# Kernel tuning notes

Measured on AMD Instinct MI355X. Metric: run time of the kernel, lower is better.

Reference implementation:

```python
import jax, jax.numpy as jnp
import numpy as np

N, D_IN, D_OUT = 8192, 512, 512


def setup_inputs() -> dict:
    key = jax.random.key(0)
    ks = jax.random.split(key, 8)
    scale_in = 1.0 / np.sqrt(D_IN)
    scale_cat = 1.0 / np.sqrt(2 * D_OUT)
    return {
        "x": jax.random.normal(ks[0], (N, D_IN), dtype=jnp.float32),
        "adj": jax.random.randint(ks[1], (N, N), 0, 2, dtype=jnp.int32),
        "W_self": jax.random.uniform(ks[2], (D_IN, D_OUT), jnp.float32, -scale_in, scale_in),
        "b_self": jax.random.uniform(ks[3], (D_OUT,), jnp.float32, -scale_in, scale_in),
        "W_nb": jax.random.uniform(ks[4], (D_IN, D_OUT), jnp.float32, -scale_in, scale_in),
        "b_nb": jax.random.uniform(ks[5], (D_OUT,), jnp.float32, -scale_in, scale_in),
        "W_comb": jax.random.uniform(ks[6], (2 * D_OUT, D_OUT), jnp.float32, -scale_cat, scale_cat),
        "b_comb": jax.random.uniform(ks[7], (D_OUT,), jnp.float32, -scale_cat, scale_cat),
    }


def reference(x, adj, W_self, b_self, W_nb, b_nb, W_comb, b_comb):
    # Vectorized equivalent of the per-node loop:
    # neighbors_i = where(adj[i] > 0); agg_i = mean(x[neighbors_i]) (zeros if none)
    mask = (adj > 0).astype(x.dtype)              # [N, N]
    deg = jnp.sum(mask, axis=1, keepdims=True)    # [N, 1]
    # sum over neighbors is mask @ x; dividing by max(deg,1) yields zeros when deg==0
    agg = (mask @ x) / jnp.maximum(deg, 1.0)      # [N, D_IN]
    self_f = x @ W_self + b_self                  # [N, D_OUT]
    nb_f = agg @ W_nb + b_nb                      # [N, D_OUT]
    combined = jnp.concatenate([self_f, nb_f], axis=-1)  # [N, 2*D_OUT]
    out = combined @ W_comb + b_comb              # [N, D_OUT]
    return jax.nn.relu(out)
```

## Files before the change

### kernel.cpp

```cpp
#include <hip/hip_runtime.h>


using short8 = __attribute__((ext_vector_type(8))) short;
using f32x4  = __attribute__((ext_vector_type(4))) float;

typedef unsigned short U16;
typedef unsigned int   U32;

__device__ __forceinline__ U16 f2bf(float f) {
  U32 u = __float_as_uint(f);
  u = (u + 0x7fffu + ((u >> 16) & 1u)) >> 16;
  return (U16)u;
}
__device__ __forceinline__ U32 pack2bf(float a, float b) {
  return (U32)f2bf(a) | ((U32)f2bf(b) << 16);
}

__global__ void GraphSAGELayer_773094114149_kernel(
    int phase,
    const float* __restrict__ x,     const int* __restrict__ adj,
    const float* __restrict__ Wself, const float* __restrict__ bself,
    const float* __restrict__ Wnb,   const float* __restrict__ bnb,
    const float* __restrict__ Wcomb, const float* __restrict__ bcomb,
    U16* __restrict__ xT, U16* __restrict__ xbf, U16* __restrict__ aggp,
    U16* __restrict__ Wt, float* __restrict__ cbias, float* __restrict__ outp)
{
  __shared__ __align__(16) unsigned char smem[27648];
  const int tid = threadIdx.x;

  if (phase == 0) {
    U16* tl = (U16*)smem;
    const int n0 = blockIdx.x * 64;
    const int m0 = blockIdx.y * 64;
    const int r  = tid >> 2;
    const int cq = (tid & 3) * 16;

    const float* src = x + (size_t)(m0 + r) * 512 + n0 + cq;
    float v[16];
    for (int i = 0; i < 16; i += 4) {
      float4 f = *(const float4*)(src + i);
      v[i] = f.x; v[i+1] = f.y; v[i+2] = f.z; v[i+3] = f.w;
    }
    U32 pk[8];
    for (int i = 0; i < 8; ++i) pk[i] = pack2bf(v[2*i], v[2*i+1]);

    U16* dst = xbf + (size_t)(m0 + r) * 512 + n0 + cq;
    *(uint4*)dst       = make_uint4(pk[0], pk[1], pk[2], pk[3]);
    *(uint4*)(dst + 8) = make_uint4(pk[4], pk[5], pk[6], pk[7]);

    for (int i = 0; i < 8; ++i) {
      tl[(cq + 2*i)     * 72 + r] = (U16)(pk[i] & 0xffffu);
      tl[(cq + 2*i + 1) * 72 + r] = (U16)(pk[i] >> 16);
    }
    __syncthreads();
    const int c2 = tid >> 2;
    const int mq = (tid & 3) * 16;
    uint4 o0 = *(const uint4*)&tl[c2 * 72 + mq];
    uint4 o1 = *(const uint4*)&tl[c2 * 72 + mq + 8];
    U16* dT = xT + (size_t)(n0 + c2) * 8192 + m0 + mq;
    *(uint4*)dT       = o0;
    *(uint4*)(dT + 8) = o1;
    return;
  }

  if (phase == 1) {
    if (blockIdx.x >= 256) {
      int n = (int)(blockIdx.x - 256) * 256 + tid;
      float acc = bcomb[n];
      for (int j = 0; j < 512; ++j) {
        acc += bself[j] * Wcomb[(size_t)j * 512 + n];
        acc += bnb[j]   * Wcomb[(size_t)(512 + j) * 512 + n];
      }
      cbias[n] = acc;
      return;
    }
    const int half = blockIdx.x >> 7;
    const int k0   = (blockIdx.x & 127) * 4;
    const float* Wsrc = half ? Wnb : Wself;
    const int woff = half * 512;

    float* wsf = (float*)smem;
    {
      int idx = tid * 8;
      *(float4*)&wsf[idx]     = *(const float4*)&Wsrc[(size_t)(k0 + (idx >> 9)) * 512 + (idx & 511)];
      *(float4*)&wsf[idx + 4] = *(const float4*)&Wsrc[(size_t)(k0 + ((idx+4) >> 9)) * 512 + ((idx+4) & 511)];
    }
    __syncthreads();

    float a[8] = {0,0,0,0,0,0,0,0};
    for (int j = 0; j < 512; ++j) {
      float wc0 = Wcomb[(size_t)(woff + j) * 512 + tid];
      float wc1 = Wcomb[(size_t)(woff + j) * 512 + tid + 256];
      float s0 = wsf[j], s1 = wsf[512 + j], s2 = wsf[1024 + j], s3 = wsf[1536 + j];
      a[0] += s0 * wc0;  a[4] += s0 * wc1;
      a[1] += s1 * wc0;  a[5] += s1 * wc1;
      a[2] += s2 * wc0;  a[6] += s2 * wc1;
      a[3] += s3 * wc0;  a[7] += s3 * wc1;
    }
    U16* w0 = Wt + (size_t)tid * 1024 + woff + k0;
    U16* w1 = Wt + (size_t)(tid + 256) * 1024 + woff + k0;
    for (int q = 0; q < 4; ++q) { w0[q] = f2bf(a[q]); w1[q] = f2bf(a[4 + q]); }
    return;
  }

  const int lane = tid & 63;
  const int wave = tid >> 6;
  const int wm = (wave & 1) * 32;
  const int wn = (wave >> 1) * 64;
  const int nBase = blockIdx.x * 128;
  const int mBase = blockIdx.y * 64;

  if (phase == 2) {
    U16* As = (U16*)smem;
    U16* Bs = (U16*)(smem + 9216);
    float* degp = (float*)(smem + 9216 + 16384);
    float* degs = degp + 256;

    const int arow = tid >> 2;
    const int* aptr = adj + (size_t)(mBase + arow) * 8192 + (tid & 3) * 16;
    U16* awr = &As[arow * 72 + (tid & 3) * 16];

    const U16* bgp[4]; U16* blp[4];
    for (int i = 0; i < 4; ++i) {
      int c  = i * 256 + tid;
      int nr = c >> 3;
      int gc = c & 7;
      bgp[i] = xT + (size_t)(nBase + nr) * 8192 + gc * 8;
      blp[i] = &Bs[nr * 64 + ((gc ^ (nr & 7)) * 8)];
    }

    f32x4 acc[2][4];
    for (int a = 0; a < 2; ++a)
      for (int b = 0; b < 4; ++b) acc[a][b] = (f32x4){0.f, 0.f, 0.f, 0.f};

    U32 degAcc = 0;

    int4 a0 = ((const int4*)aptr)[0];
    int4 a1 = ((const int4*)aptr)[1];
    int4 a2 = ((const int4*)aptr)[2];
    int4 a3 = ((const int4*)aptr)[3];
    uint4 bv0 = *(const uint4*)(bgp[0]);
    uint4 bv1 = *(const uint4*)(bgp[1]);
    uint4 bv2 = *(const uint4*)(bgp[2]);
    uint4 bv3 = *(const uint4*)(bgp[3]);

    for (int it = 0; it < 128; ++it) {
      __syncthreads();

      *(uint4*)blp[0] = bv0;
      *(uint4*)blp[1] = bv1;
      *(uint4*)blp[2] = bv2;
      *(uint4*)blp[3] = bv3;

      U32 p0 = (U32)a0.x | ((U32)a0.y << 16);
      U32 p1 = (U32)a0.z | ((U32)a0.w << 16);
      U32 p2 = (U32)a1.x | ((U32)a1.y << 16);
      U32 p3 = (U32)a1.z | ((U32)a1.w << 16);
      U32 p4 = (U32)a2.x | ((U32)a2.y << 16);
      U32 p5 = (U32)a2.z | ((U32)a2.w << 16);
      U32 p6 = (U32)a3.x | ((U32)a3.y << 16);
      U32 p7 = (U32)a3.z | ((U32)a3.w << 16);
      degAcc += p0 + p1 + p2 + p3 + p4 + p5 + p6 + p7;
      const U32 ONE = 0x3F80u;
      *(uint4*)awr       = make_uint4(p0 * ONE, p1 * ONE, p2 * ONE, p3 * ONE);
      *(uint4*)(awr + 8) = make_uint4(p4 * ONE, p5 * ONE, p6 * ONE, p7 * ONE);

      __syncthreads();

      if (it + 1 < 128) {
        const int k1 = (it + 1) * 64;
        aptr += 64;
        a0 = ((const int4*)aptr)[0];
        a1 = ((const int4*)aptr)[1];
        a2 = ((const int4*)aptr)[2];
        a3 = ((const int4*)aptr)[3];
        bv0 = *(const uint4*)(bgp[0] + k1);
        bv1 = *(const uint4*)(bgp[1] + k1);
        bv2 = *(const uint4*)(bgp[2] + k1);
        bv3 = *(const uint4*)(bgp[3] + k1);
      }

      for (int s = 0; s < 2; ++s) {
        short8 af[2], bfr[4];
        const int kb = s * 64 + ((lane >> 4) * 16);
        for (int tm = 0; tm < 2; ++tm) {
          int m = wm + tm * 16 + (lane & 15);
          af[tm] = *(const short8*)((const char*)As + m * 144 + kb);
        }
        const int g = s * 4 + (lane >> 4);
        for (int tn = 0; tn < 4; ++tn) {
          int n = wn + tn * 16 + (lane & 15);
          bfr[tn] = *(const short8*)((const char*)Bs + n * 128 + ((g ^ (n & 7)) * 16));
        }
        for (int tm = 0; tm < 2; ++tm)
          for (int tn = 0; tn < 4; ++tn)
            acc[tm][tn] = __builtin_amdgcn_mfma_f32_16x16x32_bf16(
                af[tm], bfr[tn], acc[tm][tn], 0, 0, 0);
      }
    }

    int cnt = (int)((degAcc & 0xffffu) + (degAcc >> 16));
    degp[arow * 4 + (tid & 3)] = (float)cnt;
    __syncthreads();
    if (tid < 64)
      degs[tid] = fmaxf(degp[tid*4] + degp[tid*4+1] + degp[tid*4+2] + degp[tid*4+3], 1.0f);
    __syncthreads();

    for (int tm = 0; tm < 2; ++tm) {
      int rb = wm + tm * 16 + ((lane >> 4) * 4);
      for (int r = 0; r < 4; ++r) {
        float inv = 1.0f / degs[rb + r];
        for (int tn = 0; tn < 4; ++tn) {
          int n = nBase + wn + tn * 16 + (lane & 15);
          aggp[(size_t)(mBase + rb + r) * 512 + n] = f2bf(acc[tm][tn][r] * inv);
        }
      }
    }
    return;
  }

  {
    U16* As2 = (U16*)smem;
    U16* Bs2 = (U16*)(smem + 8192);

    size_t arowoff[2]; U16* alp[2];
    for (int i = 0; i < 2; ++i) {
      int c  = i * 256 + tid;
      int mr = c >> 3;
      int gc = c & 7;
      arowoff[i] = (size_t)(mBase + mr) * 512 + gc * 8;
      alp[i] = &As2[mr * 64 + ((gc ^ (mr & 7)) * 8)];
    }
    const U16* bgp[4]; U16* blp[4];
    for (int i = 0; i < 4; ++i) {
      int c  = i * 256 + tid;
      int nr = c >> 3;
      int gc = c & 7;
      bgp[i] = Wt + (size_t)(nBase + nr) * 1024 + gc * 8;
      blp[i] = &Bs2[nr * 64 + ((gc ^ (nr & 7)) * 8)];
    }

    f32x4 acc[2][4];
    for (int a = 0; a < 2; ++a)
      for (int b = 0; b < 4; ++b) acc[a][b] = (f32x4){0.f, 0.f, 0.f, 0.f};

    uint4 av0 = *(const uint4*)(xbf + arowoff[0]);
    uint4 av1 = *(const uint4*)(xbf + arowoff[1]);
    uint4 bv0 = *(const uint4*)(bgp[0]);
    uint4 bv1 = *(const uint4*)(bgp[1]);
    uint4 bv2 = *(const uint4*)(bgp[2]);
    uint4 bv3 = *(const uint4*)(bgp[3]);

    for (int it = 0; it < 16; ++it) {
      __syncthreads();
      *(uint4*)alp[0] = av0;
      *(uint4*)alp[1] = av1;
      *(uint4*)blp[0] = bv0;
      *(uint4*)blp[1] = bv1;
      *(uint4*)blp[2] = bv2;
      *(uint4*)blp[3] = bv3;
      __syncthreads();

      if (it + 1 < 16) {
        const int k1 = (it + 1) * 64;
        const U16* ab = (k1 < 512 ? xbf : aggp) + (k1 & 511);
        av0 = *(const uint4*)(ab + arowoff[0]);
        av1 = *(const uint4*)(ab + arowoff[1]);
        bv0 = *(const uint4*)(bgp[0] + k1);
        bv1 = *(const uint4*)(bgp[1] + k1);
        bv2 = *(const uint4*)(bgp[2] + k1);
        bv3 = *(const uint4*)(bgp[3] + k1);
      }

      for (int s = 0; s < 2; ++s) {
        short8 af[2], bfr[4];
        const int g = s * 4 + (lane >> 4);
        for (int tm = 0; tm < 2; ++tm) {
          int m = wm + tm * 16 + (lane & 15);
          af[tm] = *(const short8*)((const char*)As2 + m * 128 + ((g ^ (m & 7)) * 16));
        }
        for (int tn = 0; tn < 4; ++tn) {
          int n = wn + tn * 16 + (lane & 15);
          bfr[tn] = *(const short8*)((const char*)Bs2 + n * 128 + ((g ^ (n & 7)) * 16));
        }
        for (int tm = 0; tm < 2; ++tm)
          for (int tn = 0; tn < 4; ++tn)
            acc[tm][tn] = __builtin_amdgcn_mfma_f32_16x16x32_bf16(
                af[tm], bfr[tn], acc[tm][tn], 0, 0, 0);
      }
    }

    float bias[4];
    for (int tn = 0; tn < 4; ++tn)
      bias[tn] = cbias[nBase + wn + tn * 16 + (lane & 15)];

    for (int tm = 0; tm < 2; ++tm) {
      int rb = wm + tm * 16 + ((lane >> 4) * 4);
      for (int tn = 0; tn < 4; ++tn) {
        int n = nBase + wn + tn * 16 + (lane & 15);
        for (int r = 0; r < 4; ++r) {
          float v = fmaxf(acc[tm][tn][r] + bias[tn], 0.0f);
          outp[(size_t)(mBase + rb + r) * 512 + n] = v;
        }
      }
    }
  }
}

extern "C" void kernel_launch(void* const* d_in, const int* in_sizes, int n_in,
                              void* d_out, int out_size, void* d_ws, size_t ws_size,
                              hipStream_t stream) {
  (void)in_sizes; (void)n_in; (void)out_size; (void)ws_size;

  const float* x     = (const float*)d_in[0];
  const int*   adj   = (const int*)d_in[1];
  const float* Wself = (const float*)d_in[2];
  const float* bself = (const float*)d_in[3];
  const float* Wnb   = (const float*)d_in[4];
  const float* bnb   = (const float*)d_in[5];
  const float* Wcomb = (const float*)d_in[6];
  const float* bcomb = (const float*)d_in[7];
  float* out = (float*)d_out;

  char* ws = (char*)d_ws;
  U16*   xT    = (U16*)(ws);
  U16*   xbf   = (U16*)(ws + 8388608);
  U16*   aggp  = (U16*)(ws + 16777216);
  U16*   Wt    = (U16*)(ws + 25165824);
  float* cbias = (float*)(ws + 26214400);

#define ARGS(P) (P), x, adj, Wself, bself, Wnb, bnb, Wcomb, bcomb, xT, xbf, aggp, Wt, cbias, out
  GraphSAGELayer_773094114149_kernel<<<dim3(8, 128), 256, 0, stream>>>(ARGS(0));
  GraphSAGELayer_773094114149_kernel<<<dim3(258),    256, 0, stream>>>(ARGS(1));
  GraphSAGELayer_773094114149_kernel<<<dim3(4, 128), 256, 0, stream>>>(ARGS(2));
  GraphSAGELayer_773094114149_kernel<<<dim3(4, 128), 256, 0, stream>>>(ARGS(3));
#undef ARGS
}
```

Baseline: 605.0 us.

## Bit-pack adjacency once and stream bitmask into the aggregation GEMM

A new prologue reads the int32 adjacency once, compacts each row into a 64-bit ballot bitmask, and stores the inverse degree. The aggregation GEMM then expands bits into bf16 ones in shared memory instead of re-reading the full int32 matrix in every column block. The K tile doubles to 128 and the launches shrink from four to three by merging the prep phases. The final GEMM converts x to bf16 on the fly instead of reading a separate bf16 copy. The cost is an extra bitmask buffer, a larger dynamic shared-memory footprint in the aggregation kernel, and bit-expansion work inside the inner loop.

```diff
diff --git a/kernel.cpp b/kernel.cpp
--- a/kernel.cpp
+++ b/kernel.cpp
@@ -6,6 +6,7 @@
 
 typedef unsigned short U16;
 typedef unsigned int   U32;
+typedef unsigned long long U64;
 
 __device__ __forceinline__ U16 f2bf(float f) {
   U32 u = __float_as_uint(f);
@@ -22,197 +23,202 @@
     const float* __restrict__ Wself, const float* __restrict__ bself,
     const float* __restrict__ Wnb,   const float* __restrict__ bnb,
     const float* __restrict__ Wcomb, const float* __restrict__ bcomb,
-    U16* __restrict__ xT, U16* __restrict__ xbf, U16* __restrict__ aggp,
-    U16* __restrict__ Wt, float* __restrict__ cbias, float* __restrict__ outp)
+    U16* __restrict__ xT, U16* __restrict__ aggp, U64* __restrict__ bits,
+    float* __restrict__ invdeg, U16* __restrict__ Wt,
+    float* __restrict__ cbias, float* __restrict__ outp)
 {
-  __shared__ __align__(16) unsigned char smem[27648];
+  extern __shared__ __align__(16) unsigned char smem[];
   const int tid = threadIdx.x;
 
   if (phase == 0) {
-    U16* tl = (U16*)smem;
-    const int n0 = blockIdx.x * 64;
-    const int m0 = blockIdx.y * 64;
-    const int r  = tid >> 2;
-    const int cq = (tid & 3) * 16;
-
-    const float* src = x + (size_t)(m0 + r) * 512 + n0 + cq;
-    float v[16];
-    for (int i = 0; i < 16; i += 4) {
-      float4 f = *(const float4*)(src + i);
-      v[i] = f.x; v[i+1] = f.y; v[i+2] = f.z; v[i+3] = f.w;
-    }
-    U32 pk[8];
-    for (int i = 0; i < 8; ++i) pk[i] = pack2bf(v[2*i], v[2*i+1]);
-
-    U16* dst = xbf + (size_t)(m0 + r) * 512 + n0 + cq;
-    *(uint4*)dst       = make_uint4(pk[0], pk[1], pk[2], pk[3]);
-    *(uint4*)(dst + 8) = make_uint4(pk[4], pk[5], pk[6], pk[7]);
-
-    for (int i = 0; i < 8; ++i) {
-      tl[(cq + 2*i)     * 72 + r] = (U16)(pk[i] & 0xffffu);
-      tl[(cq + 2*i + 1) * 72 + r] = (U16)(pk[i] >> 16);
-    }
-    __syncthreads();
-    const int c2 = tid >> 2;
-    const int mq = (tid & 3) * 16;
-    uint4 o0 = *(const uint4*)&tl[c2 * 72 + mq];
-    uint4 o1 = *(const uint4*)&tl[c2 * 72 + mq + 8];
-    U16* dT = xT + (size_t)(n0 + c2) * 8192 + m0 + mq;
-    *(uint4*)dT       = o0;
-    *(uint4*)(dT + 8) = o1;
-    return;
-  }
-
-  if (phase == 1) {
-    if (blockIdx.x >= 256) {
-      int n = (int)(blockIdx.x - 256) * 256 + tid;
-      float acc = bcomb[n];
+    if (blockIdx.x < 8192) {
+      const int row = blockIdx.x;
+      const int wv = tid >> 6, ln = tid & 63;
+      const int* arow = adj + (size_t)row * 8192 + wv * 2048;
+      U64* brow = bits + (size_t)row * 128 + wv * 32;
+      float* sdeg = (float*)smem;
+      int dsum = 0;
+#pragma unroll 4
+      for (int p = 0; p < 32; ++p) {
+        int v = arow[p * 64 + ln];
+        U64 mask = __ballot(v > 0);
+        dsum += (int)__popcll(mask);
+        if (ln == 0) brow[p] = mask;
+      }
+      if (ln == 0) sdeg[wv] = (float)dsum;
+      __syncthreads();
+      if (tid == 0)
+        invdeg[row] = 1.0f / fmaxf(sdeg[0] + sdeg[1] + sdeg[2] + sdeg[3], 1.0f);
+      return;
+    }
+    if (blockIdx.x < 9216) {
+      const int b = blockIdx.x - 8192;
+      const int n0 = (b & 7) * 64;
+      const int m0 = (b >> 3) * 64;
+      U16* tl = (U16*)smem;
+      const int r  = tid >> 2;
+      const int cq = (tid & 3) * 16;
+      const float* src = x + (size_t)(m0 + r) * 512 + n0 + cq;
+      U32 pk[8];
+#pragma unroll
+      for (int i = 0; i < 8; ++i) {
+        float2 f = *(const float2*)(src + 2 * i);
+        pk[i] = pack2bf(f.x, f.y);
+      }
+#pragma unroll
+      for (int i = 0; i < 8; ++i) {
+        tl[(cq + 2*i)     * 72 + r] = (U16)(pk[i] & 0xffffu);
+        tl[(cq + 2*i + 1) * 72 + r] = (U16)(pk[i] >> 16);
+      }
+      __syncthreads();
+      const int c2 = tid >> 2;
+      const int mq = (tid & 3) * 16;
+      uint4 o0 = *(const uint4*)&tl[c2 * 72 + mq];
+      uint4 o1 = *(const uint4*)&tl[c2 * 72 + mq + 8];
+      U16* dT = xT + (size_t)(n0 + c2) * 8192 + m0 + mq;
+      *(uint4*)dT       = o0;
+      *(uint4*)(dT + 8) = o1;
+      return;
+    }
+    {
+      const int b = blockIdx.x - 9216;
+      if (b >= 256) {
+        int n = (b - 256) * 256 + tid;
+        float acc = bcomb[n];
+        for (int j = 0; j < 512; ++j) {
+          acc += bself[j] * Wcomb[(size_t)j * 512 + n];
+          acc += bnb[j]   * Wcomb[(size_t)(512 + j) * 512 + n];
+        }
+        cbias[n] = acc;
+        return;
+      }
+      const int half = b >> 7;
+      const int k0   = (b & 127) * 4;
+      const float* Wsrc = half ? Wnb : Wself;
+      const int woff = half * 512;
+      float* wsf = (float*)smem;
+      {
+        int idx = tid * 8;
+        *(float4*)&wsf[idx]     = *(const float4*)&Wsrc[(size_t)(k0 + (idx >> 9)) * 512 + (idx & 511)];
+        *(float4*)&wsf[idx + 4] = *(const float4*)&Wsrc[(size_t)(k0 + ((idx+4) >> 9)) * 512 + ((idx+4) & 511)];
+      }
+      __syncthreads();
+      float a[8] = {0,0,0,0,0,0,0,0};
       for (int j = 0; j < 512; ++j) {
-        acc += bself[j] * Wcomb[(size_t)j * 512 + n];
-        acc += bnb[j]   * Wcomb[(size_t)(512 + j) * 512 + n];
-      }
-      cbias[n] = acc;
+        float wc0 = Wcomb[(size_t)(woff + j) * 512 + tid];
+        float wc1 = Wcomb[(size_t)(woff + j) * 512 + tid + 256];
+        float s0 = wsf[j], s1 = wsf[512 + j], s2 = wsf[1024 + j], s3 = wsf[1536 + j];
+        a[0] += s0 * wc0;  a[4] += s0 * wc1;
+        a[1] += s1 * wc0;  a[5] += s1 * wc1;
+        a[2] += s2 * wc0;  a[6] += s2 * wc1;
+        a[3] += s3 * wc0;  a[7] += s3 * wc1;
+      }
+      U16* w0 = Wt + (size_t)tid * 1024 + woff + k0;
+      U16* w1 = Wt + (size_t)(tid + 256) * 1024 + woff + k0;
+      for (int q = 0; q < 4; ++q) { w0[q] = f2bf(a[q]); w1[q] = f2bf(a[4 + q]); }
       return;
     }
-    const int half = blockIdx.x >> 7;
-    const int k0   = (blockIdx.x & 127) * 4;
-    const float* Wsrc = half ? Wnb : Wself;
-    const int woff = half * 512;
-
-    float* wsf = (float*)smem;
-    {
-      int idx = tid * 8;
-      *(float4*)&wsf[idx]     = *(const float4*)&Wsrc[(size_t)(k0 + (idx >> 9)) * 512 + (idx & 511)];
-      *(float4*)&wsf[idx + 4] = *(const float4*)&Wsrc[(size_t)(k0 + ((idx+4) >> 9)) * 512 + ((idx+4) & 511)];
-    }
-    __syncthreads();
-
-    float a[8] = {0,0,0,0,0,0,0,0};
-    for (int j = 0; j < 512; ++j) {
-      float wc0 = Wcomb[(size_t)(woff + j) * 512 + tid];
-      float wc1 = Wcomb[(size_t)(woff + j) * 512 + tid + 256];
-      float s0 = wsf[j], s1 = wsf[512 + j], s2 = wsf[1024 + j], s3 = wsf[1536 + j];
-      a[0] += s0 * wc0;  a[4] += s0 * wc1;
-      a[1] += s1 * wc0;  a[5] += s1 * wc1;
-      a[2] += s2 * wc0;  a[6] += s2 * wc1;
-      a[3] += s3 * wc0;  a[7] += s3 * wc1;
-    }
-    U16* w0 = Wt + (size_t)tid * 1024 + woff + k0;
-    U16* w1 = Wt + (size_t)(tid + 256) * 1024 + woff + k0;
-    for (int q = 0; q < 4; ++q) { w0[q] = f2bf(a[q]); w1[q] = f2bf(a[4 + q]); }
-    return;
   }
 
   const int lane = tid & 63;
   const int wave = tid >> 6;
+  const int quad = lane >> 4;
   const int wm = (wave & 1) * 32;
   const int wn = (wave >> 1) * 64;
   const int nBase = blockIdx.x * 128;
   const int mBase = blockIdx.y * 64;
 
-  if (phase == 2) {
-    U16* As = (U16*)smem;
-    U16* Bs = (U16*)(smem + 9216);
-    float* degp = (float*)(smem + 9216 + 16384);
-    float* degs = degp + 256;
-
-    const int arow = tid >> 2;
-    const int* aptr = adj + (size_t)(mBase + arow) * 8192 + (tid & 3) * 16;
-    U16* awr = &As[arow * 72 + (tid & 3) * 16];
-
-    const U16* bgp[4]; U16* blp[4];
-    for (int i = 0; i < 4; ++i) {
+  if (phase == 1) {
+    U16* Aa = (U16*)smem;
+    U16* Bb = (U16*)(smem + 17408);
+    const U32* bits32 = (const U32*)bits;
+
+    const int r  = tid >> 2;
+    const int qt = tid & 3;
+    const U32* abase = bits32 + (size_t)(mBase + r) * 256 + qt;
+    U16* awr = Aa + r * 136 + qt * 32;
+
+    const U16* bgp[8]; U16* blp[8];
+#pragma unroll
+    for (int i = 0; i < 8; ++i) {
       int c  = i * 256 + tid;
-      int nr = c >> 3;
-      int gc = c & 7;
-      bgp[i] = xT + (size_t)(nBase + nr) * 8192 + gc * 8;
-      blp[i] = &Bs[nr * 64 + ((gc ^ (nr & 7)) * 8)];
+      int nr = c >> 4;
+      int gk = c & 15;
+      bgp[i] = xT + (size_t)(nBase + nr) * 8192 + gk * 8;
+      blp[i] = Bb + nr * 128 + ((gk ^ (nr & 15)) * 8);
     }
 
     f32x4 acc[2][4];
+#pragma unroll
     for (int a = 0; a < 2; ++a)
+#pragma unroll
       for (int b = 0; b < 4; ++b) acc[a][b] = (f32x4){0.f, 0.f, 0.f, 0.f};
 
-    U32 degAcc = 0;
-
-    int4 a0 = ((const int4*)aptr)[0];
-    int4 a1 = ((const int4*)aptr)[1];
-    int4 a2 = ((const int4*)aptr)[2];
-    int4 a3 = ((const int4*)aptr)[3];
-    uint4 bv0 = *(const uint4*)(bgp[0]);
-    uint4 bv1 = *(const uint4*)(bgp[1]);
-    uint4 bv2 = *(const uint4*)(bgp[2]);
-    uint4 bv3 = *(const uint4*)(bgp[3]);
-
-    for (int it = 0; it < 128; ++it) {
-      __syncthreads();
-
-      *(uint4*)blp[0] = bv0;
-      *(uint4*)blp[1] = bv1;
-      *(uint4*)blp[2] = bv2;
-      *(uint4*)blp[3] = bv3;
-
-      U32 p0 = (U32)a0.x | ((U32)a0.y << 16);
-      U32 p1 = (U32)a0.z | ((U32)a0.w << 16);
-      U32 p2 = (U32)a1.x | ((U32)a1.y << 16);
-      U32 p3 = (U32)a1.z | ((U32)a1.w << 16);
-      U32 p4 = (U32)a2.x | ((U32)a2.y << 16);
-      U32 p5 = (U32)a2.z | ((U32)a2.w << 16);
-      U32 p6 = (U32)a3.x | ((U32)a3.y << 16);
-      U32 p7 = (U32)a3.z | ((U32)a3.w << 16);
-      degAcc += p0 + p1 + p2 + p3 + p4 + p5 + p6 + p7;
-      const U32 ONE = 0x3F80u;
-      *(uint4*)awr       = make_uint4(p0 * ONE, p1 * ONE, p2 * ONE, p3 * ONE);
-      *(uint4*)(awr + 8) = make_uint4(p4 * ONE, p5 * ONE, p6 * ONE, p7 * ONE);
-
-      __syncthreads();
-
-      if (it + 1 < 128) {
-        const int k1 = (it + 1) * 64;
-        aptr += 64;
-        a0 = ((const int4*)aptr)[0];
-        a1 = ((const int4*)aptr)[1];
-        a2 = ((const int4*)aptr)[2];
-        a3 = ((const int4*)aptr)[3];
-        bv0 = *(const uint4*)(bgp[0] + k1);
-        bv1 = *(const uint4*)(bgp[1] + k1);
-        bv2 = *(const uint4*)(bgp[2] + k1);
-        bv3 = *(const uint4*)(bgp[3] + k1);
-      }
-
-      for (int s = 0; s < 2; ++s) {
+    U32 abits = abase[0];
+    uint4 bv[8];
+#pragma unroll
+    for (int i = 0; i < 8; ++i) bv[i] = *(const uint4*)(bgp[i]);
+
+    for (int it = 0; it < 64; ++it) {
+      __syncthreads();
+
+#pragma unroll
+      for (int i = 0; i < 8; ++i) *(uint4*)blp[i] = bv[i];
+
+      U32 o[16];
+#pragma unroll
+      for (int j = 0; j < 16; ++j) {
+        U32 t2 = (abits >> (2 * j)) & 3u;
+        o[j] = ((t2 | (t2 << 15)) & 0x10001u) * 0x3F80u;
+      }
+      *(uint4*)(awr)      = make_uint4(o[0],  o[1],  o[2],  o[3]);
+      *(uint4*)(awr + 8)  = make_uint4(o[4],  o[5],  o[6],  o[7]);
+      *(uint4*)(awr + 16) = make_uint4(o[8],  o[9],  o[10], o[11]);
+      *(uint4*)(awr + 24) = make_uint4(o[12], o[13], o[14], o[15]);
+
+      __syncthreads();
+
+      if (it + 1 < 64) {
+        const int k1 = (it + 1) * 128;
+        abits = abase[(it + 1) * 4];
+#pragma unroll
+        for (int i = 0; i < 8; ++i) bv[i] = *(const uint4*)(bgp[i] + k1);
+      }
+
+#pragma unroll
+      for (int s = 0; s < 4; ++s) {
         short8 af[2], bfr[4];
-        const int kb = s * 64 + ((lane >> 4) * 16);
+        const int kb = s * 64 + quad * 16;
+#pragma unroll
         for (int tm = 0; tm < 2; ++tm) {
           int m = wm + tm * 16 + (lane & 15);
-          af[tm] = *(const short8*)((const char*)As + m * 144 + kb);
-        }
-        const int g = s * 4 + (lane >> 4);
+          af[tm] = *(const short8*)((const char*)Aa + m * 272 + kb);
+        }
+        const int g = s * 4 + quad;
+#pragma unroll
         for (int tn = 0; tn < 4; ++tn) {
           int n = wn + tn * 16 + (lane & 15);
-          bfr[tn] = *(const short8*)((const char*)Bs + n * 128 + ((g ^ (n & 7)) * 16));
-        }
+          bfr[tn] = *(const short8*)((const char*)Bb + n * 256 + ((g ^ (n & 15)) * 16));
+        }
+#pragma unroll
         for (int tm = 0; tm < 2; ++tm)
+#pragma unroll
           for (int tn = 0; tn < 4; ++tn)
             acc[tm][tn] = __builtin_amdgcn_mfma_f32_16x16x32_bf16(
                 af[tm], bfr[tn], acc[tm][tn], 0, 0, 0);
       }
     }
 
-    int cnt = (int)((degAcc & 0xffffu) + (degAcc >> 16));
-    degp[arow * 4 + (tid & 3)] = (float)cnt;
-    __syncthreads();
-    if (tid < 64)
-      degs[tid] = fmaxf(degp[tid*4] + degp[tid*4+1] + degp[tid*4+2] + degp[tid*4+3], 1.0f);
-    __syncthreads();
-
+#pragma unroll
     for (int tm = 0; tm < 2; ++tm) {
-      int rb = wm + tm * 16 + ((lane >> 4) * 4);
-      for (int r = 0; r < 4; ++r) {
-        float inv = 1.0f / degs[rb + r];
+      int rb = wm + tm * 16 + quad * 4;
+#pragma unroll
+      for (int rr = 0; rr < 4; ++rr) {
+        float inv = invdeg[mBase + rb + rr];
+#pragma unroll
         for (int tn = 0; tn < 4; ++tn) {
           int n = nBase + wn + tn * 16 + (lane & 15);
-          aggp[(size_t)(mBase + rb + r) * 512 + n] = f2bf(acc[tm][tn][r] * inv);
+          aggp[(size_t)(mBase + rb + rr) * 512 + n] = f2bf(acc[tm][tn][rr] * inv);
         }
       }
     }
@@ -223,67 +229,88 @@
     U16* As2 = (U16*)smem;
     U16* Bs2 = (U16*)(smem + 8192);
 
-    size_t arowoff[2]; U16* alp[2];
+    int amr[2], agc[2]; U16* alp[2];
+#pragma unroll
     for (int i = 0; i < 2; ++i) {
       int c  = i * 256 + tid;
-      int mr = c >> 3;
-      int gc = c & 7;
-      arowoff[i] = (size_t)(mBase + mr) * 512 + gc * 8;
-      alp[i] = &As2[mr * 64 + ((gc ^ (mr & 7)) * 8)];
+      amr[i] = c >> 3;
+      agc[i] = c & 7;
+      alp[i] = As2 + amr[i] * 64 + ((agc[i] ^ (amr[i] & 7)) * 8);
     }
     const U16* bgp[4]; U16* blp[4];
+#pragma unroll
     for (int i = 0; i < 4; ++i) {
       int c  = i * 256 + tid;
       int nr = c >> 3;
       int gc = c & 7;
       bgp[i] = Wt + (size_t)(nBase + nr) * 1024 + gc * 8;
-      blp[i] = &Bs2[nr * 64 + ((gc ^ (nr & 7)) * 8)];
+      blp[i] = Bs2 + nr * 64 + ((gc ^ (nr & 7)) * 8);
     }
 
     f32x4 acc[2][4];
+#pragma unroll
     for (int a = 0; a < 2; ++a)
+#pragma unroll
       for (int b = 0; b < 4; ++b) acc[a][b] = (f32x4){0.f, 0.f, 0.f, 0.f};
 
-    uint4 av0 = *(const uint4*)(xbf + arowoff[0]);
-    uint4 av1 = *(const uint4*)(xbf + arowoff[1]);
-    uint4 bv0 = *(const uint4*)(bgp[0]);
-    uint4 bv1 = *(const uint4*)(bgp[1]);
-    uint4 bv2 = *(const uint4*)(bgp[2]);
-    uint4 bv3 = *(const uint4*)(bgp[3]);
+    uint4 av[2], bv[4];
+#pragma unroll
+    for (int i = 0; i < 2; ++i) {
+      const float* ap = x + (size_t)(mBase + amr[i]) * 512 + agc[i] * 8;
+      float4 f0 = *(const float4*)ap;
+      float4 f1 = *(const float4*)(ap + 4);
+      av[i] = make_uint4(pack2bf(f0.x,f0.y), pack2bf(f0.z,f0.w),
+                         pack2bf(f1.x,f1.y), pack2bf(f1.z,f1.w));
+    }
+#pragma unroll
+    for (int i = 0; i < 4; ++i) bv[i] = *(const uint4*)(bgp[i]);
 
     for (int it = 0; it < 16; ++it) {
       __syncthreads();
-      *(uint4*)alp[0] = av0;
-      *(uint4*)alp[1] = av1;
-      *(uint4*)blp[0] = bv0;
-      *(uint4*)blp[1] = bv1;
-      *(uint4*)blp[2] = bv2;
-      *(uint4*)blp[3] = bv3;
+#pragma unroll
+      for (int i = 0; i < 2; ++i) *(uint4*)alp[i] = av[i];
+#pragma unroll
+      for (int i = 0; i < 4; ++i) *(uint4*)blp[i] = bv[i];
       __syncthreads();
 
       if (it + 1 < 16) {
-        const int k1 = (it + 1) * 64;
-        const U16* ab = (k1 < 512 ? xbf : aggp) + (k1 & 511);
-        av0 = *(const uint4*)(ab + arowoff[0]);
-        av1 = *(const uint4*)(ab + arowoff[1]);
-        bv0 = *(const uint4*)(bgp[0] + k1);
-        bv1 = *(const uint4*)(bgp[1] + k1);
-        bv2 = *(const uint4*)(bgp[2] + k1);
-        bv3 = *(const uint4*)(bgp[3] + k1);
-      }
-
+        const int it1 = it + 1;
+        if (it1 < 8) {
+#pragma unroll
+          for (int i = 0; i < 2; ++i) {
+            const float* ap = x + (size_t)(mBase + amr[i]) * 512 + it1 * 64 + agc[i] * 8;
+            float4 f0 = *(const float4*)ap;
+            float4 f1 = *(const float4*)(ap + 4);
+            av[i] = make_uint4(pack2bf(f0.x,f0.y), pack2bf(f0.z,f0.w),
+                               pack2bf(f1.x,f1.y), pack2bf(f1.z,f1.w));
+          }
+        } else {
+#pragma unroll
+          for (int i = 0; i < 2; ++i)
+            av[i] = *(const uint4*)(aggp + (size_t)(mBase + amr[i]) * 512 +
+                                    (it1 - 8) * 64 + agc[i] * 8);
+        }
+#pragma unroll
+        for (int i = 0; i < 4; ++i) bv[i] = *(const uint4*)(bgp[i] + it1 * 64);
+      }
+
+#pragma unroll
       for (int s = 0; s < 2; ++s) {
         short8 af[2], bfr[4];
-        const int g = s * 4 + (lane >> 4);
+        const int g = s * 4 + quad;
+#pragma unroll
         for (int tm = 0; tm < 2; ++tm) {
           int m = wm + tm * 16 + (lane & 15);
           af[tm] = *(const short8*)((const char*)As2 + m * 128 + ((g ^ (m & 7)) * 16));
         }
+#pragma unroll
         for (int tn = 0; tn < 4; ++tn) {
           int n = wn + tn * 16 + (lane & 15);
           bfr[tn] = *(const short8*)((const char*)Bs2 + n * 128 + ((g ^ (n & 7)) * 16));
         }
+#pragma unroll
         for (int tm = 0; tm < 2; ++tm)
+#pragma unroll
           for (int tn = 0; tn < 4; ++tn)
             acc[tm][tn] = __builtin_amdgcn_mfma_f32_16x16x32_bf16(
                 af[tm], bfr[tn], acc[tm][tn], 0, 0, 0);
@@ -291,16 +318,20 @@
     }
 
     float bias[4];
+#pragma unroll
     for (int tn = 0; tn < 4; ++tn)
       bias[tn] = cbias[nBase + wn + tn * 16 + (lane & 15)];
 
+#pragma unroll
     for (int tm = 0; tm < 2; ++tm) {
-      int rb = wm + tm * 16 + ((lane >> 4) * 4);
+      int rb = wm + tm * 16 + quad * 4;
+#pragma unroll
       for (int tn = 0; tn < 4; ++tn) {
         int n = nBase + wn + tn * 16 + (lane & 15);
-        for (int r = 0; r < 4; ++r) {
-          float v = fmaxf(acc[tm][tn][r] + bias[tn], 0.0f);
-          outp[(size_t)(mBase + rb + r) * 512 + n] = v;
+#pragma unroll
+        for (int rr = 0; rr < 4; ++rr) {
+          float v = fmaxf(acc[tm][tn][rr] + bias[tn], 0.0f);
+          outp[(size_t)(mBase + rb + rr) * 512 + n] = v;
         }
       }
     }
@@ -323,16 +354,17 @@
   float* out = (float*)d_out;
 
   char* ws = (char*)d_ws;
-  U16*   xT    = (U16*)(ws);
-  U16*   xbf   = (U16*)(ws + 8388608);
-  U16*   aggp  = (U16*)(ws + 16777216);
-  U16*   Wt    = (U16*)(ws + 25165824);
-  float* cbias = (float*)(ws + 26214400);
-
-#define ARGS(P) (P), x, adj, Wself, bself, Wnb, bnb, Wcomb, bcomb, xT, xbf, aggp, Wt, cbias, out
-  GraphSAGELayer_773094114149_kernel<<<dim3(8, 128), 256, 0, stream>>>(ARGS(0));
-  GraphSAGELayer_773094114149_kernel<<<dim3(258),    256, 0, stream>>>(ARGS(1));
-  GraphSAGELayer_773094114149_kernel<<<dim3(4, 128), 256, 0, stream>>>(ARGS(2));
-  GraphSAGELayer_773094114149_kernel<<<dim3(4, 128), 256, 0, stream>>>(ARGS(3));
+  U16*   xT     = (U16*)(ws);
+  U16*   aggp   = (U16*)(ws + 8388608);
+  U64*   bits   = (U64*)(ws + 16777216);
+  U16*   Wt     = (U16*)(ws + 25165824);
+  float* cbias  = (float*)(ws + 26214400);
+  float* invdeg = (float*)(ws + 26216448);
+
+#define ARGS(P) (P), x, adj, Wself, bself, Wnb, bnb, Wcomb, bcomb, \
+                xT, aggp, bits, invdeg, Wt, cbias, out
+  GraphSAGELayer_773094114149_kernel<<<dim3(9474),   256,  9216, stream>>>(ARGS(0));
+  GraphSAGELayer_773094114149_kernel<<<dim3(4, 128), 256, 50176, stream>>>(ARGS(1));
+  GraphSAGELayer_773094114149_kernel<<<dim3(4, 128), 256, 24576, stream>>>(ARGS(2));
 #undef ARGS
 }
```

New measurement: 838.9 us. 1.39x slower.
